# Optimization experiments

Measured on AMD Instinct MI355X. Metric: run time of the kernel, lower is better.

## Reference

```python
import jax, jax.numpy as jnp
import numpy as np

NUM_DIRECTIONS = 64
NUM_STEPS = 64
D = 64
NEG_INF = -1e9  # matches the original's -inf sentinel of 1e9


def _sample_directions(n):
    # Mirrors WeightedEulerCurve._obtainDirection with np.random.seed(4)
    np.random.seed(4)
    out = []
    for _ in range(n):
        phi = np.random.uniform(0, np.pi * 2)
        costheta = np.random.uniform(-1, 1)
        theta = np.arccos(costheta)
        out.append([np.sin(theta) * np.cos(phi), np.sin(theta) * np.sin(phi), np.cos(theta)])
    return np.asarray(out, dtype=np.float32)


def setup_inputs() -> dict:
    key = jax.random.key(0)
    # strictly positive -> dense cubical complex (every voxel is a vertex,
    # every adjacent pair an edge, etc.), matching torch.nonzero on x>0
    x = jax.random.uniform(key, (D, D, D), dtype=jnp.float32) + 1e-3
    dirs = jnp.asarray(_sample_directions(NUM_DIRECTIONS))  # (K, 3)
    return {"x": x, "dirs": dirs}


def _pairmax(a, axis):
    n = a.shape[axis]
    return jnp.maximum(jax.lax.slice_in_dim(a, 0, n - 1, axis=axis),
                       jax.lax.slice_in_dim(a, 1, n, axis=axis))


def _curve_contrib(heights, vals, intervals):
    # heights: (K, N) per-direction simplex heights; vals: (N,) shared weights
    K = heights.shape[0]
    idx = jnp.argsort(heights, axis=-1)
    sorted_h = jnp.take_along_axis(heights, idx, axis=-1)
    sorted_v = jnp.take(vals, idx)                                    # (K, N)
    csum = jnp.concatenate([jnp.zeros((K, 1), heights.dtype),
                            jnp.cumsum(sorted_v, axis=-1)], axis=-1)  # (K, N+1)
    padded_h = jnp.concatenate([jnp.full((K, 1), NEG_INF, heights.dtype),
                                sorted_h], axis=-1)                   # (K, N+1)
    ptr = jax.vmap(lambda h: jnp.searchsorted(h, intervals, side='right'))(padded_h) - 1
    return jnp.take_along_axis(csum, ptr, axis=-1)                    # (K, num_intervals)


def _wect(x, dirs, num_steps):
    d = x.shape[0]
    K = dirs.shape[0]
    r = jnp.arange(d, dtype=x.dtype)
    d0, d1, d2 = dirs[:, 0], dirs[:, 1], dirs[:, 2]
    # vertex heights per direction: H[k,i,j,l] = d0*i + d1*j + d2*l
    H = (d0[:, None, None, None] * r[:, None, None]
         + d1[:, None, None, None] * r[None, :, None]
         + d2[:, None, None, None] * r[None, None, :])
    p0, p1, p2 = (jax.nn.relu(d0)[:, None], jax.nn.relu(d1)[:, None], jax.nn.relu(d2)[:, None])

    min_h = -(3.0 ** 0.5) * d
    dh = (-2.0 * min_h) / num_steps
    intervals = jnp.asarray(min_h + dh * np.arange(num_steps + 1), dtype=x.dtype)

    # vertices
    vh = H.reshape(K, -1)
    vv = x.reshape(-1)

    # edges along each axis: max over the 2 endpoints -> base height + relu(d_axis)
    eh = jnp.concatenate([
        H[:, :-1].reshape(K, -1) + p0,
        H[:, :, :-1].reshape(K, -1) + p1,
        H[:, :, :, :-1].reshape(K, -1) + p2], axis=1)
    ev = jnp.concatenate([
        _pairmax(x, 0).reshape(-1),
        _pairmax(x, 1).reshape(-1),
        _pairmax(x, 2).reshape(-1)])

    # squares spanning axis pairs (1,2), (0,2), (0,1): max over 4 corners
    sh = jnp.concatenate([
        H[:, :, :-1, :-1].reshape(K, -1) + p1 + p2,
        H[:, :-1, :, :-1].reshape(K, -1) + p0 + p2,
        H[:, :-1, :-1, :].reshape(K, -1) + p0 + p1], axis=1)
    sv = jnp.concatenate([
        _pairmax(_pairmax(x, 1), 2).reshape(-1),
        _pairmax(_pairmax(x, 0), 2).reshape(-1),
        _pairmax(_pairmax(x, 0), 1).reshape(-1)])

    # cubes: max over 8 corners
    ch = H[:, :-1, :-1, :-1].reshape(K, -1) + p0 + p1 + p2
    cv = _pairmax(_pairmax(_pairmax(x, 0), 1), 2).reshape(-1)

    v = _curve_contrib(vh, vv, intervals)
    e = _curve_contrib(eh, ev, intervals)
    s = _curve_contrib(sh, sv, intervals)
    c = _curve_contrib(ch, cv, intervals)
    return v - e + s - c  # (K, num_steps + 1)


def reference(x, dirs):
    return _wect(x, dirs, NUM_STEPS)
```

## Files before the change

### kernel.cpp

```cpp
#include <hip/hip_runtime.h>
#include <math.h>

#define NDIRS 64
#define NBIN 65
#define WIN 21
#define WROW (WIN*64)
#define STAGEF 512
#define THREADS 256
#define WPB 4
#define NBLK 1024
#define ROWF (NDIRS*NBIN)
#define MROWS 64

static constexpr float INV = 0.28867513459481287f;

__global__ __launch_bounds__(THREADS) void wect_hist(
    const float* __restrict__ x, const float* __restrict__ dirs,
    float* __restrict__ accum) {
  __shared__ float histw[WPB * WROW];
  __shared__ float stage[WPB * STAGEF];
  __shared__ int   b0s[WPB * 64];
  const int tid = threadIdx.x;
  const int lane = tid & 63;
  const int wid  = tid >> 6;

  float4* h4 = (float4*)histw;
  for (int idx = tid; idx < WPB * WROW / 4; idx += THREADS)
    h4[idx] = make_float4(0.f, 0.f, 0.f, 0.f);
  __syncthreads();

  const float D0 = dirs[3*lane+0] * INV;
  const float D1 = dirs[3*lane+1] * INV;
  const float D2 = dirs[3*lane+2] * INV;
  const float Q1 = fmaxf(D0, 0.f);
  const float Q2 = fmaxf(D1, 0.f);
  const float Q3 = fmaxf(D2, 0.f);
  const float Q4 = Q2 + Q3;
  const float Q5 = Q1 + Q3;
  const float Q6 = Q1 + Q2;
  const float Q7 = Q1 + Q2 + Q3;

  float* __restrict__ myhw = histw + wid * WROW + lane;
  float4* __restrict__ mystage = (float4*)(stage + wid * STAGEF);

  {
    const int strip = blockIdx.x * WPB + wid;
    const int i = strip >> 6, j = strip & 63;
    const int l = lane;
    const float* p = x + (strip << 6) + l;
    const int dL = (l < 63) ? 1 : 0;
    const int dJ = (j < 63) ? 64 : 0;
    const int dI = (i < 63) ? 4096 : 0;
    const bool iv = dI != 0, jv = dJ != 0, lv = dL != 0;

    const float x000 = p[0],       x001 = p[dL];
    const float x010 = p[dJ],      x011 = p[dJ+dL];
    const float x100 = p[dI],      x101 = p[dI+dL];
    const float x110 = p[dI+dJ],   x111 = p[dI+dJ+dL];

    const float e0m = fmaxf(x000, x100);
    const float e1m = fmaxf(x000, x010);
    const float e2m = fmaxf(x000, x001);
    const float s12 = fmaxf(fmaxf(e1m, x001), x011);
    const float s02 = fmaxf(fmaxf(e0m, x001), x101);
    const float s01 = fmaxf(fmaxf(e0m, x010), x110);
    const float cc  = fmaxf(fmaxf(s01, fmaxf(x001, x101)), fmaxf(x011, x111));

    const float v1 = iv ? -e0m : 0.f;
    const float v2 = jv ? -e1m : 0.f;
    const float v3 = lv ? -e2m : 0.f;
    const float v4 = (jv && lv) ? s12 : 0.f;
    const float v5 = (iv && lv) ? s02 : 0.f;
    const float v6 = (iv && jv) ? s01 : 0.f;
    const float v7 = (iv && jv && lv) ? -cc : 0.f;
    const float T  = x000 + v1+v2+v3+v4+v5+v6+v7;

    mystage[2*lane]     = make_float4(T,  v1, v2, v3);
    mystage[2*lane + 1] = make_float4(v4, v5, v6, v7);

    const float u0 = (float)i * D0 + (float)j * D1;

    const float u63  = fmaf(63.f, D2, u0);
    const int   base = (int)ceilf(fminf(u0, u63));
    b0s[wid * 64 + lane] = base + 32;

    int   wb = (int)ceilf(u0) - base;
    float r0 = 0.f, r1 = 0.f;

    #pragma unroll 8
    for (int t = 0; t < 64; ++t) {
      const float4 A = mystage[2*t];
      const float4 B = mystage[2*t + 1];
      const float u  = fmaf((float)t, D2, u0);
      const float bf = ceilf(u);
      const float fr = bf - u;
      const int   wbn = (int)bf - base;
      const int   d   = wbn - wb;
      const float r0s = (d == 0) ? r0 : ((d > 0) ? r1 : 0.f);
      const float r1s = (d == 0) ? r1 : ((d > 0) ? 0.f : r0);
      float S = 0.f;
      S += (Q1 > fr) ? A.y : 0.f;
      S += (Q2 > fr) ? A.z : 0.f;
      S += (Q3 > fr) ? A.w : 0.f;
      S += (Q4 > fr) ? B.x : 0.f;
      S += (Q5 > fr) ? B.y : 0.f;
      S += (Q6 > fr) ? B.z : 0.f;
      S += (Q7 > fr) ? B.w : 0.f;
      r0 = r0s + (A.x - S);
      r1 = r1s + S;
      wb = wbn;
      float* a = myhw + (wbn << 6);
      a[0]  = r0;
      a[64] = r1;
    }
  }

  __syncthreads();
  float* __restrict__ obase = accum + blockIdx.x * ROWF;
  const int k = tid & 63;
  const int b00 = b0s[0*64 + k], b01 = b0s[1*64 + k],
            b02 = b0s[2*64 + k], b03 = b0s[3*64 + k];
  for (int z = tid; z < ROWF; z += THREADS) {
    const int c = z >> 6;
    float v = 0.f;
    const int w0 = c - b00;
    if ((unsigned)w0 < WIN) v += histw[0*WROW + (w0 << 6) + k];
    const int w1 = c - b01;
    if ((unsigned)w1 < WIN) v += histw[1*WROW + (w1 << 6) + k];
    const int w2 = c - b02;
    if ((unsigned)w2 < WIN) v += histw[2*WROW + (w2 << 6) + k];
    const int w3 = c - b03;
    if ((unsigned)w3 < WIN) v += histw[3*WROW + (w3 << 6) + k];
    obase[z] = v;
  }
}

__global__ __launch_bounds__(256) void wect_reduceA(
    const float* __restrict__ accum, float* __restrict__ mid) {
  const int q = blockIdx.x * 256 + threadIdx.x;
  if (q >= MROWS * ROWF) return;
  const int g = q / ROWF, z = q - g * ROWF;
  float v = 0.f;
  #pragma unroll
  for (int m = 0; m < NBLK / MROWS; ++m)
    v += accum[(g * (NBLK / MROWS) + m) * ROWF + z];
  mid[g * ROWF + z] = v;
}

__global__ __launch_bounds__(512) void wect_scan(
    const float* __restrict__ mid, float* __restrict__ out) {
  __shared__ float red[8 * NBIN];
  __shared__ float s[NBIN];
  const int k = blockIdx.x, tid = threadIdx.x;
  for (int z = tid; z < 8 * NBIN; z += 512) {
    const int g = z / NBIN, c = z - g * NBIN;
    float v = 0.f;
    #pragma unroll
    for (int r = g; r < MROWS; r += 8) v += mid[r * ROWF + (c << 6) + k];
    red[z] = v;
  }
  __syncthreads();
  if (tid < NBIN) {
    float v = 0.f;
    #pragma unroll
    for (int gg = 0; gg < 8; ++gg) v += red[gg * NBIN + tid];
    s[tid] = v;
  }
  __syncthreads();
  for (int off = 1; off < NBIN; off <<= 1) {
    float a = 0.f;
    if (tid < NBIN && tid >= off) a = s[tid - off];
    __syncthreads();
    if (tid < NBIN && tid >= off) s[tid] += a;
    __syncthreads();
  }
  if (tid < NBIN) out[k * NBIN + tid] = s[tid];
}

extern "C" void kernel_launch(void* const* d_in, const int* in_sizes, int n_in,
                              void* d_out, int out_size, void* d_ws, size_t ws_size,
                              hipStream_t stream) {
  const float* x = (const float*)d_in[0];
  const float* dirs = (const float*)d_in[1];
  float* out = (float*)d_out;
  float* accum = (float*)d_ws;
  float* mid = accum + NBLK * ROWF;

  wect_hist<<<NBLK, THREADS, 0, stream>>>(x, dirs, accum);
  wect_reduceA<<<(MROWS * ROWF + 255) / 256, 256, 0, stream>>>(accum, mid);
  wect_scan<<<NDIRS, 512, 0, stream>>>(mid, out);
}
```

Measured before the change: 91.16 us.

## Broadcast voxel weights via readlane and orient histogram window by direction sign

Drops the per-wave LDS staging buffer. Each step of the loop now broadcasts the eight per-voxel weights from lane t with readlane, which replaces two float4 LDS reads per iteration. The sliding two-bin register state is reworked into a monotone write scheme: the window index is mirrored for descending directions, only one LDS store is issued per step, and the last open bin is written after the loop. The reduction phase now applies a per-direction sign when mapping bins back, so more index arithmetic and scalar readlane traffic are traded for fewer LDS accesses.

Measured after the change: 100.3 us. +10.1%, slower.

```diff
diff --git a/kernel.cpp b/kernel.cpp
--- a/kernel.cpp
+++ b/kernel.cpp
@@ -5,7 +5,6 @@
 #define NBIN 65
 #define WIN 21
 #define WROW (WIN*64)
-#define STAGEF 512
 #define THREADS 256
 #define WPB 4
 #define NBLK 1024
@@ -14,12 +13,16 @@
 
 static constexpr float INV = 0.28867513459481287f;
 
+__device__ __forceinline__ float rdlane(float v, int t) {
+  return __int_as_float(__builtin_amdgcn_readlane(__float_as_int(v), t));
+}
+
 __global__ __launch_bounds__(THREADS) void wect_hist(
     const float* __restrict__ x, const float* __restrict__ dirs,
     float* __restrict__ accum) {
   __shared__ float histw[WPB * WROW];
-  __shared__ float stage[WPB * STAGEF];
   __shared__ int   b0s[WPB * 64];
+  __shared__ int   sgs[WPB * 64];
   const int tid = threadIdx.x;
   const int lane = tid & 63;
   const int wid  = tid >> 6;
@@ -41,7 +44,6 @@
   const float Q7 = Q1 + Q2 + Q3;
 
   float* __restrict__ myhw = histw + wid * WROW + lane;
-  float4* __restrict__ mystage = (float4*)(stage + wid * STAGEF);
 
   {
     const int strip = blockIdx.x * WPB + wid;
@@ -66,53 +68,61 @@
     const float s01 = fmaxf(fmaxf(e0m, x010), x110);
     const float cc  = fmaxf(fmaxf(s01, fmaxf(x001, x101)), fmaxf(x011, x111));
 
-    const float v1 = iv ? -e0m : 0.f;
-    const float v2 = jv ? -e1m : 0.f;
-    const float v3 = lv ? -e2m : 0.f;
-    const float v4 = (jv && lv) ? s12 : 0.f;
-    const float v5 = (iv && lv) ? s02 : 0.f;
-    const float v6 = (iv && jv) ? s01 : 0.f;
-    const float v7 = (iv && jv && lv) ? -cc : 0.f;
-    const float T  = x000 + v1+v2+v3+v4+v5+v6+v7;
-
-    mystage[2*lane]     = make_float4(T,  v1, v2, v3);
-    mystage[2*lane + 1] = make_float4(v4, v5, v6, v7);
+    const float g1 = iv ? -e0m : 0.f;
+    const float g2 = jv ? -e1m : 0.f;
+    const float g3 = lv ? -e2m : 0.f;
+    const float g4 = (jv && lv) ? s12 : 0.f;
+    const float g5 = (iv && lv) ? s02 : 0.f;
+    const float g6 = (iv && jv) ? s01 : 0.f;
+    const float g7 = (iv && jv && lv) ? -cc : 0.f;
+    const float gT = x000 + g1+g2+g3+g4+g5+g6+g7;
 
     const float u0 = (float)i * D0 + (float)j * D1;
 
-    const float u63  = fmaf(63.f, D2, u0);
-    const int   base = (int)ceilf(fminf(u0, u63));
-    b0s[wid * 64 + lane] = base + 32;
-
-    int   wb = (int)ceilf(u0) - base;
-    float r0 = 0.f, r1 = 0.f;
+    const bool desc = (D2 < 0.f);
+    const int  ib0  = (int)ceilf(u0);
+    b0s[wid*64 + lane] = desc ? (ib0 + 33) : (ib0 + 32);
+    sgs[wid*64 + lane] = desc ? -1 : 1;
+
+    int   w  = 0;
+    float rW = 0.f, rO = 0.f;
 
     #pragma unroll 8
     for (int t = 0; t < 64; ++t) {
-      const float4 A = mystage[2*t];
-      const float4 B = mystage[2*t + 1];
+      const float At = rdlane(gT, t);
+      const float A1 = rdlane(g1, t);
+      const float A2 = rdlane(g2, t);
+      const float A3 = rdlane(g3, t);
+      const float A4 = rdlane(g4, t);
+      const float A5 = rdlane(g5, t);
+      const float A6 = rdlane(g6, t);
+      const float A7 = rdlane(g7, t);
+
       const float u  = fmaf((float)t, D2, u0);
       const float bf = ceilf(u);
       const float fr = bf - u;
-      const int   wbn = (int)bf - base;
-      const int   d   = wbn - wb;
-      const float r0s = (d == 0) ? r0 : ((d > 0) ? r1 : 0.f);
-      const float r1s = (d == 0) ? r1 : ((d > 0) ? 0.f : r0);
+      const int   wa = (int)bf - ib0;
+      const int   wn = desc ? -wa : wa;
+      const bool  adv = (wn != w);
+      rW = adv ? rO : rW;
+      rO = adv ? 0.f : rO;
+      w  = wn;
+
       float S = 0.f;
-      S += (Q1 > fr) ? A.y : 0.f;
-      S += (Q2 > fr) ? A.z : 0.f;
-      S += (Q3 > fr) ? A.w : 0.f;
-      S += (Q4 > fr) ? B.x : 0.f;
-      S += (Q5 > fr) ? B.y : 0.f;
-      S += (Q6 > fr) ? B.z : 0.f;
-      S += (Q7 > fr) ? B.w : 0.f;
-      r0 = r0s + (A.x - S);
-      r1 = r1s + S;
-      wb = wbn;
-      float* a = myhw + (wbn << 6);
-      a[0]  = r0;
-      a[64] = r1;
+      S += (Q1 > fr) ? A1 : 0.f;
+      S += (Q2 > fr) ? A2 : 0.f;
+      S += (Q3 > fr) ? A3 : 0.f;
+      S += (Q4 > fr) ? A4 : 0.f;
+      S += (Q5 > fr) ? A5 : 0.f;
+      S += (Q6 > fr) ? A6 : 0.f;
+      S += (Q7 > fr) ? A7 : 0.f;
+      const float TmS = At - S;
+
+      rW += desc ? S : TmS;
+      rO += desc ? TmS : S;
+      myhw[w << 6] = rW;
     }
+    myhw[(w + 1) << 6] = rO;
   }
 
   __syncthreads();
@@ -120,16 +130,18 @@
   const int k = tid & 63;
   const int b00 = b0s[0*64 + k], b01 = b0s[1*64 + k],
             b02 = b0s[2*64 + k], b03 = b0s[3*64 + k];
+  const int s00 = sgs[0*64 + k], s01i = sgs[1*64 + k],
+            s02i = sgs[2*64 + k], s03 = sgs[3*64 + k];
   for (int z = tid; z < ROWF; z += THREADS) {
     const int c = z >> 6;
     float v = 0.f;
-    const int w0 = c - b00;
+    const int w0 = s00 * (c - b00);
     if ((unsigned)w0 < WIN) v += histw[0*WROW + (w0 << 6) + k];
-    const int w1 = c - b01;
+    const int w1 = s01i * (c - b01);
     if ((unsigned)w1 < WIN) v += histw[1*WROW + (w1 << 6) + k];
-    const int w2 = c - b02;
+    const int w2 = s02i * (c - b02);
     if ((unsigned)w2 < WIN) v += histw[2*WROW + (w2 << 6) + k];
-    const int w3 = c - b03;
+    const int w3 = s03 * (c - b03);
     if ((unsigned)w3 < WIN) v += histw[3*WROW + (w3 << 6) + k];
     obase[z] = v;
   }
```
